# Kernel optimization log

Measured on AMD Instinct MI355X. Metric: run time of the kernel, lower is better.

The kernel has to match this reference:

```python
import jax, jax.numpy as jnp
import numpy as np

H = 2048
EPS = 1e-5  # torch LayerNorm default

def layer_norm(x, g, b):
    mu = jnp.mean(x, axis=-1, keepdims=True)
    var = jnp.mean(jnp.square(x - mu), axis=-1, keepdims=True)
    return (x - mu) * jax.lax.rsqrt(var + EPS) * g + b

def setup_inputs() -> dict:
    key = jax.random.key(0)
    ks = jax.random.split(key, 5)
    bound = 1.0 / np.sqrt(H)  # torch Linear default init range
    x = jax.random.normal(ks[0], (8192, H), dtype=jnp.float32)
    W1 = jax.random.uniform(ks[1], (H, H), jnp.float32, -bound, bound)
    b1 = jax.random.uniform(ks[2], (H,), jnp.float32, -bound, bound)
    W2 = jax.random.uniform(ks[3], (H, H), jnp.float32, -bound, bound)
    b2 = jax.random.uniform(ks[4], (H,), jnp.float32, -bound, bound)
    g1 = jnp.ones((H,), jnp.float32); be1 = jnp.zeros((H,), jnp.float32)
    g2 = jnp.ones((H,), jnp.float32); be2 = jnp.zeros((H,), jnp.float32)
    return {"x": x, "W1": W1, "b1": b1, "W2": W2, "b2": b2,
            "g1": g1, "be1": be1, "g2": g2, "be2": be2}

def reference(x, W1, b1, W2, b2, g1, be1, g2, be2):
    # ln1 -> linear1 -> relu -> (dropout p=0) -> ln2 -> linear2 -> (dropout p=0) -> +x -> relu
    out = layer_norm(x, g1, be1)
    out = jax.nn.relu(out @ W1.T + b1)
    out = layer_norm(out, g2, be2)
    out = out @ W2.T + b2
    return jax.nn.relu(out + x)
```

## Files before the change

kernel.cpp:

```cpp
#include <hip/hip_runtime.h>
#include <hip/hip_bf16.h>

#define H_DIM 2048
#define LN_EPS 1e-5f

typedef __bf16 bf16_t;
typedef __bf16 bf16x4 __attribute__((ext_vector_type(4)));
typedef __bf16 bf16x8 __attribute__((ext_vector_type(8)));
typedef float f32x4 __attribute__((ext_vector_type(4)));

__device__ __forceinline__ void async_copy16(const void* g, void* l) {
    __builtin_amdgcn_global_load_lds((const __attribute__((address_space(1))) void*)g,
                                     (__attribute__((address_space(3))) void*)l,
                                     16, 0, 0);
}

#define FENCE() asm volatile("" ::: "memory")
#define BARRIER() do { FENCE(); __builtin_amdgcn_s_barrier(); FENCE(); } while (0)

__global__ __launch_bounds__(256) void cast_w_kernel(const float* __restrict__ w,
                                                     bf16_t* __restrict__ o, int n4) {
    int i = blockIdx.x * 256 + threadIdx.x;
    if (i < n4) {
        float4 v = reinterpret_cast<const float4*>(w)[i];
        bf16x4 r;
        r[0] = (bf16_t)v.x; r[1] = (bf16_t)v.y; r[2] = (bf16_t)v.z; r[3] = (bf16_t)v.w;
        reinterpret_cast<bf16x4*>(o)[i] = r;
    }
}

__global__ __launch_bounds__(256) void ln_f32_v2(const float* __restrict__ in,
                                                 const float* __restrict__ g,
                                                 const float* __restrict__ b,
                                                 bf16_t* __restrict__ out) {
    const int l = threadIdx.x & 63, w = threadIdx.x >> 6;
    const size_t row = (size_t)blockIdx.x * 4 + w;
    const float* xr = in + row * H_DIM;
    float4 v[8];
    #pragma unroll
    for (int k = 0; k < 8; ++k) v[k] = reinterpret_cast<const float4*>(xr)[l + k * 64];
    float s = 0.f, s2 = 0.f;
    #pragma unroll
    for (int k = 0; k < 8; ++k) {
        s  += v[k].x + v[k].y + v[k].z + v[k].w;
        s2 += v[k].x * v[k].x + v[k].y * v[k].y + v[k].z * v[k].z + v[k].w * v[k].w;
    }
    #pragma unroll
    for (int off = 32; off > 0; off >>= 1) {
        s  += __shfl_down(s,  off, 64);
        s2 += __shfl_down(s2, off, 64);
    }
    s  = __shfl(s,  0, 64);
    s2 = __shfl(s2, 0, 64);
    float mu   = s * (1.f / H_DIM);
    float rstd = rsqrtf(s2 * (1.f / H_DIM) - mu * mu + LN_EPS);
    bf16_t* orow = out + row * H_DIM;
    #pragma unroll
    for (int k = 0; k < 8; ++k) {
        int c = l + k * 64;
        float4 gv = reinterpret_cast<const float4*>(g)[c];
        float4 bv = reinterpret_cast<const float4*>(b)[c];
        bf16x4 y;
        y[0] = (bf16_t)((v[k].x - mu) * rstd * gv.x + bv.x);
        y[1] = (bf16_t)((v[k].y - mu) * rstd * gv.y + bv.y);
        y[2] = (bf16_t)((v[k].z - mu) * rstd * gv.z + bv.z);
        y[3] = (bf16_t)((v[k].w - mu) * rstd * gv.w + bv.w);
        reinterpret_cast<bf16x4*>(orow)[c] = y;
    }
}

__global__ __launch_bounds__(256) void ln_bf16_v2(const bf16_t* __restrict__ in,
                                                  const float* __restrict__ g,
                                                  const float* __restrict__ b,
                                                  bf16_t* __restrict__ out) {
    const int l = threadIdx.x & 63, w = threadIdx.x >> 6;
    const size_t row = (size_t)blockIdx.x * 4 + w;
    const bf16_t* xr = in + row * H_DIM;
    bf16x8 xv[4];
    #pragma unroll
    for (int k = 0; k < 4; ++k) xv[k] = reinterpret_cast<const bf16x8*>(xr)[l + k * 64];
    float vv[32];
    #pragma unroll
    for (int k = 0; k < 4; ++k)
        #pragma unroll
        for (int j = 0; j < 8; ++j) vv[k * 8 + j] = (float)xv[k][j];
    float s = 0.f, s2 = 0.f;
    #pragma unroll
    for (int e = 0; e < 32; ++e) { s += vv[e]; s2 += vv[e] * vv[e]; }
    #pragma unroll
    for (int off = 32; off > 0; off >>= 1) {
        s  += __shfl_down(s,  off, 64);
        s2 += __shfl_down(s2, off, 64);
    }
    s  = __shfl(s,  0, 64);
    s2 = __shfl(s2, 0, 64);
    float mu   = s * (1.f / H_DIM);
    float rstd = rsqrtf(s2 * (1.f / H_DIM) - mu * mu + LN_EPS);
    bf16_t* orow = out + row * H_DIM;
    #pragma unroll
    for (int k = 0; k < 4; ++k) {
        int c = l + k * 64;
        float4 g0 = reinterpret_cast<const float4*>(g)[c * 2];
        float4 g1 = reinterpret_cast<const float4*>(g)[c * 2 + 1];
        float4 b0 = reinterpret_cast<const float4*>(b)[c * 2];
        float4 b1 = reinterpret_cast<const float4*>(b)[c * 2 + 1];
        bf16x8 y;
        y[0] = (bf16_t)((vv[k*8+0] - mu) * rstd * g0.x + b0.x);
        y[1] = (bf16_t)((vv[k*8+1] - mu) * rstd * g0.y + b0.y);
        y[2] = (bf16_t)((vv[k*8+2] - mu) * rstd * g0.z + b0.z);
        y[3] = (bf16_t)((vv[k*8+3] - mu) * rstd * g0.w + b0.w);
        y[4] = (bf16_t)((vv[k*8+4] - mu) * rstd * g1.x + b1.x);
        y[5] = (bf16_t)((vv[k*8+5] - mu) * rstd * g1.y + b1.y);
        y[6] = (bf16_t)((vv[k*8+6] - mu) * rstd * g1.z + b1.z);
        y[7] = (bf16_t)((vv[k*8+7] - mu) * rstd * g1.w + b1.w);
        reinterpret_cast<bf16x8*>(orow)[c] = y;
    }
}

template<int FINAL>
__global__ __launch_bounds__(512, 2) void gemm8_kernel(
    const bf16_t* __restrict__ A,
    const bf16_t* __restrict__ B,
    const float*  __restrict__ bias,
    const float*  __restrict__ resid,
    bf16_t* __restrict__ obf,
    float*  __restrict__ of)
{
    __shared__ bf16_t sm[8 * 8192];

    const int tid = threadIdx.x;
    const int l  = tid & 63, w = tid >> 6;
    const int wm = w >> 2,  wn = w & 3;
    const int cl = l & 15,  ch = l >> 4;

    const int cpx = gridDim.x >> 3;
    const int bid = blockIdx.x;
    const int swz = (bid & 7) * cpx + (bid >> 3);
    const size_t row0 = (size_t)(swz >> 3) * 256;
    const size_t col0 = (size_t)(swz & 7) * 256;

    const bf16_t* Abase = A + row0 * H_DIM;
    const bf16_t* Bbase = B + col0 * H_DIM;

    const int rr  = w * 8 + (l >> 3);
    const int scb = (l & 7) ^ (l >> 3);
    const size_t soff  = (size_t)rr * H_DIM + scb * 8;
    const int ldsw0 = w * 512;
    const int ldsw1 = 4096 + w * 512;

    const int swx = cl & 7;
    const int cbks[2] = { ch ^ swx, (4 + ch) ^ swx };

    f32x4 acc[2][4][4] = {};

    auto STAGE = [&](const bf16_t* Gb, int kt, int half, int region) {
        const bf16_t* g = Gb + (size_t)half * (128 * H_DIM) + kt * 64 + soff;
        bf16_t* s = &sm[region * 8192];
        async_copy16(g,               s + ldsw0);
        async_copy16(g + 64 * H_DIM,  s + ldsw1);
    };
    auto RDA = [&](int buf, int mh, int m, int ks) -> bf16x8 {
        int r = mh * 64 + m * 16 + cl;
        return *(const bf16x8*)&sm[(buf * 4 + wm) * 8192 + r * 64 + cbks[ks] * 8];
    };
    auto RDB = [&](int buf, int n, int ks) -> bf16x8 {
        int r = (wn & 1) * 64 + n * 16 + cl;
        return *(const bf16x8*)&sm[(buf * 4 + 2 + (wn >> 1)) * 8192 + r * 64 + cbks[ks] * 8];
    };

    auto KTILE = [&](int t, bool stA, bool stB, int vm) {
        const int buf = t & 1;
        bf16x8 a[4], b0[4], b1[4];
        #pragma unroll
        for (int n = 0; n < 4; ++n) { b0[n] = RDB(buf, n, 0); b1[n] = RDB(buf, n, 1); }
        #pragma unroll
        for (int m = 0; m < 4; ++m) a[m] = RDA(buf, 0, m, 0);
        if (stA) STAGE(Abase, t + 1, 0, ((t + 1) & 1) * 4 + 0);
        BARRIER();
        __builtin_amdgcn_s_setprio(1);
        #pragma unroll
        for (int m = 0; m < 4; ++m)
            #pragma unroll
            for (int n = 0; n < 4; ++n)
                acc[0][m][n] = __builtin_amdgcn_mfma_f32_16x16x32_bf16(a[m], b0[n], acc[0][m][n], 0, 0, 0);
        __builtin_amdgcn_s_setprio(0);
        BARRIER();
        #pragma unroll
        for (int m = 0; m < 4; ++m) a[m] = RDA(buf, 0, m, 1);
        if (stA) STAGE(Abase, t + 1, 1, ((t + 1) & 1) * 4 + 1);
        BARRIER();
        __builtin_amdgcn_s_setprio(1);
        #pragma unroll
        for (int m = 0; m < 4; ++m)
            #pragma unroll
            for (int n = 0; n < 4; ++n)
                acc[0][m][n] = __builtin_amdgcn_mfma_f32_16x16x32_bf16(a[m], b1[n], acc[0][m][n], 0, 0, 0);
        __builtin_amdgcn_s_setprio(0);
        BARRIER();
        #pragma unroll
        for (int m = 0; m < 4; ++m) a[m] = RDA(buf, 1, m, 0);
        if (stB) STAGE(Bbase, t + 2, 0, buf * 4 + 2);
        BARRIER();
        __builtin_amdgcn_s_setprio(1);
        #pragma unroll
        for (int m = 0; m < 4; ++m)
            #pragma unroll
            for (int n = 0; n < 4; ++n)
                acc[1][m][n] = __builtin_amdgcn_mfma_f32_16x16x32_bf16(a[m], b0[n], acc[1][m][n], 0, 0, 0);
        __builtin_amdgcn_s_setprio(0);
        BARRIER();
        #pragma unroll
        for (int m = 0; m < 4; ++m) a[m] = RDA(buf, 1, m, 1);
        if (stB) STAGE(Bbase, t + 2, 1, buf * 4 + 3);
        BARRIER();
        __builtin_amdgcn_s_setprio(1);
        #pragma unroll
        for (int m = 0; m < 4; ++m)
            #pragma unroll
            for (int n = 0; n < 4; ++n)
                acc[1][m][n] = __builtin_amdgcn_mfma_f32_16x16x32_bf16(a[m], b1[n], acc[1][m][n], 0, 0, 0);
        __builtin_amdgcn_s_setprio(0);
        if (vm == 4)      asm volatile("s_waitcnt vmcnt(4)");
        else if (vm == 0) asm volatile("s_waitcnt vmcnt(0)");
        BARRIER();
    };

    STAGE(Abase, 0, 0, 0); STAGE(Abase, 0, 1, 1);
    STAGE(Bbase, 0, 0, 2); STAGE(Bbase, 0, 1, 3);
    STAGE(Bbase, 1, 0, 6); STAGE(Bbase, 1, 1, 7);
    asm volatile("s_waitcnt vmcnt(4)");
    BARRIER();

    const int NT = H_DIM / 64;
    for (int t = 0; t < NT - 2; ++t) KTILE(t, true, true, 4);
    KTILE(NT - 2, true, false, 0);
    KTILE(NT - 1, false, false, -1);

    #pragma unroll
    for (int mh = 0; mh < 2; ++mh)
        #pragma unroll
        for (int m = 0; m < 4; ++m)
            #pragma unroll
            for (int n = 0; n < 4; ++n) {
                size_t col = col0 + wn * 64 + n * 16 + cl;
                float bv = bias[col];
                #pragma unroll
                for (int j = 0; j < 4; ++j) {
                    size_t row = row0 + wm * 128 + mh * 64 + m * 16 + ch * 4 + j;
                    size_t idx = row * H_DIM + col;
                    float v = acc[mh][m][n][j] + bv;
                    if constexpr (FINAL) {
                        v += resid[idx];
                        of[idx] = fmaxf(v, 0.f);
                    } else {
                        obf[idx] = (bf16_t)fmaxf(v, 0.f);
                    }
                }
            }
}

extern "C" void kernel_launch(void* const* d_in, const int* in_sizes, int n_in,
                              void* d_out, int out_size, void* d_ws, size_t ws_size,
                              hipStream_t stream) {
    const float* x   = (const float*)d_in[0];
    const float* W1  = (const float*)d_in[1];
    const float* b1  = (const float*)d_in[2];
    const float* W2  = (const float*)d_in[3];
    const float* b2  = (const float*)d_in[4];
    const float* g1  = (const float*)d_in[5];
    const float* be1 = (const float*)d_in[6];
    const float* g2  = (const float*)d_in[7];
    const float* be2 = (const float*)d_in[8];
    float* out = (float*)d_out;

    const int M = in_sizes[0] / H_DIM;

    char* ws = (char*)d_ws;
    bf16_t* W1b = (bf16_t*)(ws);
    bf16_t* W2b = (bf16_t*)(ws + (8u << 20));
    bf16_t* lnb = (bf16_t*)(ws + (16u << 20));
    bf16_t* h1  = (bf16_t*)(ws + (48u << 20));

    const int wn4 = (H_DIM * H_DIM) / 4;
    cast_w_kernel<<<dim3((wn4 + 255) / 256), dim3(256), 0, stream>>>(W1, W1b, wn4);
    cast_w_kernel<<<dim3((wn4 + 255) / 256), dim3(256), 0, stream>>>(W2, W2b, wn4);

    ln_f32_v2<<<dim3(M / 4), dim3(256), 0, stream>>>(x, g1, be1, lnb);

    gemm8_kernel<0><<<dim3((M / 256) * 8), dim3(512), 0, stream>>>(
        lnb, W1b, b1, nullptr, h1, nullptr);

    ln_bf16_v2<<<dim3(M / 4), dim3(256), 0, stream>>>(h1, g2, be2, lnb);

    gemm8_kernel<1><<<dim3((M / 256) * 8), dim3(512), 0, stream>>>(
        lnb, W2b, b2, x, nullptr, out);
}
```

Before: 309.6 us.

## Fuse weight casts, stage GEMM1 epilogue via LDS, use bf16 residual copy

Several changes at once. The two weight-cast launches merge into one kernel. The first LayerNorm also writes a bf16 copy of x, which the final GEMM reads as its residual instead of fp32 x. GEMM1's epilogue now goes through per-wave LDS tiles so global stores become 16-byte vectors instead of scattered 2-byte writes. The k-loop is unrolled by two with fixed buffer indices, and B-fragment loads are split so fewer registers are live. The bf16 residual loses precision in the skip connection, and the extra xb write costs bandwidth in the LN kernel.

Result: faster. 302.7 us (-2.2%).

```diff
diff --git a/kernel.cpp b/kernel.cpp
--- a/kernel.cpp
+++ b/kernel.cpp
@@ -18,21 +18,26 @@
 #define FENCE() asm volatile("" ::: "memory")
 #define BARRIER() do { FENCE(); __builtin_amdgcn_s_barrier(); FENCE(); } while (0)
 
-__global__ __launch_bounds__(256) void cast_w_kernel(const float* __restrict__ w,
-                                                     bf16_t* __restrict__ o, int n4) {
+__global__ __launch_bounds__(256) void cast2_kernel(const float* __restrict__ w1,
+                                                    const float* __restrict__ w2,
+                                                    bf16_t* __restrict__ o1,
+                                                    bf16_t* __restrict__ o2) {
+    const int n4 = (H_DIM * H_DIM) / 4;
     int i = blockIdx.x * 256 + threadIdx.x;
-    if (i < n4) {
-        float4 v = reinterpret_cast<const float4*>(w)[i];
-        bf16x4 r;
-        r[0] = (bf16_t)v.x; r[1] = (bf16_t)v.y; r[2] = (bf16_t)v.z; r[3] = (bf16_t)v.w;
-        reinterpret_cast<bf16x4*>(o)[i] = r;
-    }
+    const float* src; bf16_t* dst; int j;
+    if (i < n4) { src = w1; dst = o1; j = i; }
+    else        { src = w2; dst = o2; j = i - n4; }
+    float4 v = reinterpret_cast<const float4*>(src)[j];
+    bf16x4 r;
+    r[0] = (bf16_t)v.x; r[1] = (bf16_t)v.y; r[2] = (bf16_t)v.z; r[3] = (bf16_t)v.w;
+    reinterpret_cast<bf16x4*>(dst)[j] = r;
 }
 
 __global__ __launch_bounds__(256) void ln_f32_v2(const float* __restrict__ in,
                                                  const float* __restrict__ g,
                                                  const float* __restrict__ b,
-                                                 bf16_t* __restrict__ out) {
+                                                 bf16_t* __restrict__ out,
+                                                 bf16_t* __restrict__ xb) {
     const int l = threadIdx.x & 63, w = threadIdx.x >> 6;
     const size_t row = (size_t)blockIdx.x * 4 + w;
     const float* xr = in + row * H_DIM;
@@ -55,6 +60,7 @@
     float mu   = s * (1.f / H_DIM);
     float rstd = rsqrtf(s2 * (1.f / H_DIM) - mu * mu + LN_EPS);
     bf16_t* orow = out + row * H_DIM;
+    bf16_t* xrow = xb ? xb + row * H_DIM : nullptr;
     #pragma unroll
     for (int k = 0; k < 8; ++k) {
         int c = l + k * 64;
@@ -66,6 +72,12 @@
         y[2] = (bf16_t)((v[k].z - mu) * rstd * gv.z + bv.z);
         y[3] = (bf16_t)((v[k].w - mu) * rstd * gv.w + bv.w);
         reinterpret_cast<bf16x4*>(orow)[c] = y;
+        if (xrow) {
+            bf16x4 xv;
+            xv[0] = (bf16_t)v[k].x; xv[1] = (bf16_t)v[k].y;
+            xv[2] = (bf16_t)v[k].z; xv[3] = (bf16_t)v[k].w;
+            reinterpret_cast<bf16x4*>(xrow)[c] = xv;
+        }
     }
 }
 
@@ -117,12 +129,15 @@
     }
 }
 
-template<int FINAL>
+#define LDW 88
+
+template<int FINAL, int RB>
 __global__ __launch_bounds__(512, 2) void gemm8_kernel(
     const bf16_t* __restrict__ A,
     const bf16_t* __restrict__ B,
     const float*  __restrict__ bias,
-    const float*  __restrict__ resid,
+    const float*  __restrict__ residf,
+    const bf16_t* __restrict__ residb,
     bf16_t* __restrict__ obf,
     float*  __restrict__ of)
 {
@@ -168,14 +183,13 @@
         return *(const bf16x8*)&sm[(buf * 4 + 2 + (wn >> 1)) * 8192 + r * 64 + cbks[ks] * 8];
     };
 
-    auto KTILE = [&](int t, bool stA, bool stB, int vm) {
-        const int buf = t & 1;
+    auto KT = [&](int buf, int t, bool stA, bool stB, int vm) {
         bf16x8 a[4], b0[4], b1[4];
         #pragma unroll
-        for (int n = 0; n < 4; ++n) { b0[n] = RDB(buf, n, 0); b1[n] = RDB(buf, n, 1); }
+        for (int n = 0; n < 4; ++n) b0[n] = RDB(buf, n, 0);
         #pragma unroll
         for (int m = 0; m < 4; ++m) a[m] = RDA(buf, 0, m, 0);
-        if (stA) STAGE(Abase, t + 1, 0, ((t + 1) & 1) * 4 + 0);
+        if (stA) STAGE(Abase, t + 1, 0, (buf ^ 1) * 4 + 0);
         BARRIER();
         __builtin_amdgcn_s_setprio(1);
         #pragma unroll
@@ -186,8 +200,10 @@
         __builtin_amdgcn_s_setprio(0);
         BARRIER();
         #pragma unroll
+        for (int n = 0; n < 4; ++n) b1[n] = RDB(buf, n, 1);
+        #pragma unroll
         for (int m = 0; m < 4; ++m) a[m] = RDA(buf, 0, m, 1);
-        if (stA) STAGE(Abase, t + 1, 1, ((t + 1) & 1) * 4 + 1);
+        if (stA) STAGE(Abase, t + 1, 1, (buf ^ 1) * 4 + 1);
         BARRIER();
         __builtin_amdgcn_s_setprio(1);
         #pragma unroll
@@ -231,32 +247,56 @@
     asm volatile("s_waitcnt vmcnt(4)");
     BARRIER();
 
-    const int NT = H_DIM / 64;
-    for (int t = 0; t < NT - 2; ++t) KTILE(t, true, true, 4);
-    KTILE(NT - 2, true, false, 0);
-    KTILE(NT - 1, false, false, -1);
-
-    #pragma unroll
-    for (int mh = 0; mh < 2; ++mh)
-        #pragma unroll
-        for (int m = 0; m < 4; ++m)
-            #pragma unroll
-            for (int n = 0; n < 4; ++n) {
-                size_t col = col0 + wn * 64 + n * 16 + cl;
-                float bv = bias[col];
+    for (int t = 0; t < 30; t += 2) {
+        KT(0, t,     true, true, 4);
+        KT(1, t + 1, true, true, 4);
+    }
+    KT(0, 30, true,  false, 0);
+    KT(1, 31, false, false, -1);
+
+    if constexpr (FINAL) {
+        #pragma unroll
+        for (int mh = 0; mh < 2; ++mh)
+            #pragma unroll
+            for (int m = 0; m < 4; ++m)
                 #pragma unroll
-                for (int j = 0; j < 4; ++j) {
-                    size_t row = row0 + wm * 128 + mh * 64 + m * 16 + ch * 4 + j;
-                    size_t idx = row * H_DIM + col;
-                    float v = acc[mh][m][n][j] + bv;
-                    if constexpr (FINAL) {
-                        v += resid[idx];
-                        of[idx] = fmaxf(v, 0.f);
-                    } else {
-                        obf[idx] = (bf16_t)fmaxf(v, 0.f);
+                for (int n = 0; n < 4; ++n) {
+                    size_t col = col0 + wn * 64 + n * 16 + cl;
+                    float bv = bias[col];
+                    #pragma unroll
+                    for (int j = 0; j < 4; ++j) {
+                        size_t row = row0 + wm * 128 + mh * 64 + m * 16 + ch * 4 + j;
+                        size_t idx = row * H_DIM + col;
+                        float rv = RB ? (float)residb[idx] : residf[idx];
+                        of[idx] = fmaxf(acc[mh][m][n][j] + bv + rv, 0.f);
                     }
                 }
+    } else {
+        bf16_t* wls = (bf16_t*)((char*)sm + w * (64 * LDW * 2));
+        #pragma unroll
+        for (int mh = 0; mh < 2; ++mh) {
+            #pragma unroll
+            for (int m = 0; m < 4; ++m)
+                #pragma unroll
+                for (int n = 0; n < 4; ++n) {
+                    float bv = bias[col0 + wn * 64 + n * 16 + cl];
+                    #pragma unroll
+                    for (int j = 0; j < 4; ++j) {
+                        int lr = m * 16 + ch * 4 + j;
+                        int lc = n * 16 + cl;
+                        wls[lr * LDW + lc] = (bf16_t)fmaxf(acc[mh][m][n][j] + bv, 0.f);
+                    }
+                }
+            #pragma unroll
+            for (int k = 0; k < 8; ++k) {
+                int c = l + k * 64;
+                int r = c >> 3, cb = c & 7;
+                bf16x8 vv = *(const bf16x8*)&wls[r * LDW + cb * 8];
+                size_t grow = row0 + wm * 128 + mh * 64 + r;
+                *(bf16x8*)&obf[grow * H_DIM + col0 + wn * 64 + cb * 8] = vv;
             }
+        }
+    }
 }
 
 extern "C" void kernel_launch(void* const* d_in, const int* in_sizes, int n_in,
@@ -280,18 +320,24 @@
     bf16_t* W2b = (bf16_t*)(ws + (8u << 20));
     bf16_t* lnb = (bf16_t*)(ws + (16u << 20));
     bf16_t* h1  = (bf16_t*)(ws + (48u << 20));
-
-    const int wn4 = (H_DIM * H_DIM) / 4;
-    cast_w_kernel<<<dim3((wn4 + 255) / 256), dim3(256), 0, stream>>>(W1, W1b, wn4);
-    cast_w_kernel<<<dim3((wn4 + 255) / 256), dim3(256), 0, stream>>>(W2, W2b, wn4);
-
-    ln_f32_v2<<<dim3(M / 4), dim3(256), 0, stream>>>(x, g1, be1, lnb);
-
-    gemm8_kernel<0><<<dim3((M / 256) * 8), dim3(512), 0, stream>>>(
-        lnb, W1b, b1, nullptr, h1, nullptr);
+    const bool use_xb = ws_size >= ((size_t)96 << 20);
+    bf16_t* xb  = use_xb ? (bf16_t*)(ws + (80u << 20)) : nullptr;
+
+    const int n4tot = 2 * (H_DIM * H_DIM) / 4;
+    cast2_kernel<<<dim3(n4tot / 256), dim3(256), 0, stream>>>(W1, W2, W1b, W2b);
+
+    ln_f32_v2<<<dim3(M / 4), dim3(256), 0, stream>>>(x, g1, be1, lnb, xb);
+
+    gemm8_kernel<0, 0><<<dim3((M / 256) * 8), dim3(512), 0, stream>>>(
+        lnb, W1b, b1, nullptr, nullptr, h1, nullptr);
 
     ln_bf16_v2<<<dim3(M / 4), dim3(256), 0, stream>>>(h1, g2, be2, lnb);
 
-    gemm8_kernel<1><<<dim3((M / 256) * 8), dim3(512), 0, stream>>>(
-        lnb, W2b, b2, x, nullptr, out);
-}
+    if (use_xb) {
+        gemm8_kernel<1, 1><<<dim3((M / 256) * 8), dim3(512), 0, stream>>>(
+            lnb, W2b, b2, nullptr, xb, nullptr, out);
+    } else {
+        gemm8_kernel<1, 0><<<dim3((M / 256) * 8), dim3(512), 0, stream>>>(
+            lnb, W2b, b2, x, nullptr, nullptr, out);
+    }
+}
```
